# Kernel tuning notes

Hardware: AMD Instinct MI355X
Metric: run time of the kernel (lower is better)

The kernel has to match this reference:

```python
import jax, jax.numpy as jnp
import numpy as np
from jax.scipy.special import logsumexp

T, B, N = 512, 512, 64  # time, batch, labels


def setup_inputs() -> dict:
    key = jax.random.key(0)
    k1, k2, k3, k4, k5, k6 = jax.random.split(key, 6)
    scale = 1.0 / np.sqrt(N).astype(np.float32)  # matches init.normal_(0, 1/sqrt(N))
    emit = jax.random.normal(k1, (T, B, N), jnp.float32)
    transitions = jax.random.normal(k2, (N, N), jnp.float32) * scale
    strans = jax.random.normal(k3, (N,), jnp.float32) * scale
    etrans = jax.random.normal(k4, (N,), jnp.float32) * scale
    target = jax.random.randint(k5, (T, B), 0, N)
    lengths = jax.random.randint(k6, (B,), 1, T + 1)  # at least 1 valid step
    mask = jnp.arange(T)[:, None] < lengths[None, :]  # (T, B) bool, mask[0] all True
    return {"emit": emit, "transitions": transitions, "strans": strans,
            "etrans": etrans, "target": target, "mask": mask}


def reference(emit, transitions, strans, etrans, target, mask):
    # ---- get_logZ: semiring (logsumexp) scan over time ----
    def step(alpha, xs):
        emit_i, mask_i = xs  # (B, N), (B,)
        # scores[b, j] = logsumexp_i alpha[b, i] + trans[i, j] + emit_i[b, j]
        scores = logsumexp(alpha[:, :, None] + transitions[None, :, :]
                           + emit_i[:, None, :], axis=1)
        alpha = jnp.where(mask_i[:, None], scores, alpha)
        return alpha, None

    alpha0 = emit[0] + strans  # (B, N)
    alpha, _ = jax.lax.scan(step, alpha0, (emit[1:], mask[1:]))
    logZ = logsumexp(alpha + etrans, axis=1).sum()

    # ---- score: gold-path score ----
    trans_sc = transitions[target[:-1], target[1:]]                 # (T-1, B)
    emit_sc = jnp.take_along_axis(emit, target[:, :, None], axis=2)[..., 0]  # (T, B)
    step_sc = emit_sc.at[1:].add(trans_sc)
    gold = jnp.where(mask, step_sc, 0.0).sum()
    ends = mask.sum(axis=0) - 1                                     # (B,) last valid step
    gold = gold + strans[target[0]].sum()
    gold = gold + etrans[target[ends, jnp.arange(B)]].sum()

    # negative log-likelihood (standard CRF loss = logZ - gold score)
    return logZ - gold
```

## Files before the change

kernel.cpp:

```cpp
#include <hip/hip_runtime.h>

#define TT 512
#define BB 512
#define NN 64
#define LN2F 0.69314718055994530942f

typedef _Float16 half8_t __attribute__((ext_vector_type(8)));
typedef float    f32x4   __attribute__((ext_vector_type(4)));

union AFrag { int u[4]; half8_t h; };

__device__ __forceinline__ float wave_max(float v) {
    #pragma unroll
    for (int off = 32; off > 0; off >>= 1)
        v = fmaxf(v, __shfl_xor(v, off, 64));
    return v;
}

__device__ __forceinline__ float wave_sum(float v) {
    #pragma unroll
    for (int off = 32; off > 0; off >>= 1)
        v += __shfl_xor(v, off, 64);
    return v;
}

__device__ __forceinline__ int wave_sum_i(int v) {
    #pragma unroll
    for (int off = 32; off > 0; off >>= 1)
        v += __shfl_xor(v, off, 64);
    return v;
}

__device__ __forceinline__ float bcast_lane(float v, int lane) {
    return __uint_as_float(__builtin_amdgcn_readlane(__float_as_uint(v), lane));
}

__device__ __forceinline__ void async4(const float* g, float* l) {
    __builtin_amdgcn_global_load_lds(
        (const __attribute__((address_space(1))) unsigned int*)g,
        (__attribute__((address_space(3))) unsigned int*)l,
        4, 0, 0);
}

__global__ void zero_kernel(float* __restrict__ out) {
    if (threadIdx.x == 0 && blockIdx.x == 0) out[0] = 0.0f;
}

__global__ __launch_bounds__(64) void crf_fwd_kernel(
    const float* __restrict__ emit,
    const float* __restrict__ trans,
    const float* __restrict__ strans,
    const float* __restrict__ etrans,
    const int*   __restrict__ target,
    const void*  __restrict__ maskp,
    float* __restrict__ out)
{
    const int b = blockIdx.x;
    const int k = threadIdx.x;

    __shared__ float sem[2][8][NN];

    const int*           mi32 = (const int*)maskp;
    const unsigned char* mi8  = (const unsigned char*)maskp;
    const bool bytemode = (mi32[0] == 0x01010101);

    int cnt = 0;
    #pragma unroll
    for (int i = 0; i < TT / 64; ++i) {
        const size_t tb = (size_t)(i * 64 + k) * BB + b;
        cnt += bytemode ? (mi8[tb] != 0) : (mi32[tb] != 0);
    }
    const int len = wave_sum_i(cnt);

    const int q   = k >> 4;
    const int nlo = k & 15;
    const bool bit4 = (k & 16) != 0;
    const bool bit5 = (k & 32) != 0;

    const float* ecol = emit + (size_t)b * NN + k;

    #pragma unroll
    for (int s = 0; s < 8; ++s)
        async4(ecol + (size_t)(1 + s) * BB * NN, &sem[0][s][0]);

    half8_t Bf[4][2];
    #pragma unroll
    for (int g = 0; g < 4; ++g) {
        #pragma unroll
        for (int kh = 0; kh < 2; ++kh) {
            AFrag bf;
            #pragma unroll
            for (int jp = 0; jp < 4; ++jp) {
                const int krow = 32 * kh + 8 * q + 2 * jp;
                const float e0 = 0.25f * __expf(trans[(krow + 0) * NN + 16 * g + nlo]);
                const float e1 = 0.25f * __expf(trans[(krow + 1) * NN + 16 * g + nlo]);
                bf.u[jp] = __builtin_bit_cast(int, __builtin_amdgcn_cvt_pkrtz(e0, e1));
            }
            Bf[g][kh] = bf.h;
        }
    }

    int addrs[8];
    #pragma unroll
    for (int kh = 0; kh < 2; ++kh)
        #pragma unroll
        for (int r = 0; r < 4; ++r)
            addrs[4 * kh + r] = 128 * kh + 32 * q + 8 * r;

    const f32x4 zero4 = {0.f, 0.f, 0.f, 0.f};

    const float alpha0 = ecol[0] + strans[k];
    const float m0 = bcast_lane(alpha0, 0);
    float u = __expf(alpha0 - m0);
    int e_sum = 0;

    auto do_step = [&](float wloc) {
        const float uo = __int_as_float(
            __builtin_amdgcn_mov_dpp(__float_as_int(u), 0xB1, 0xF, 0xF, true));
        const int pkv = __builtin_bit_cast(int, __builtin_amdgcn_cvt_pkrtz(u, uo));

        AFrag a0f, a1f;
        #pragma unroll
        for (int r = 0; r < 4; ++r) {
            a0f.u[r] = __builtin_amdgcn_ds_bpermute(addrs[r],     pkv);
            a1f.u[r] = __builtin_amdgcn_ds_bpermute(addrs[4 + r], pkv);
        }

        const f32x4 accA0 = __builtin_amdgcn_mfma_f32_16x16x32_f16(a0f.h, Bf[0][0], zero4, 0, 0, 0);
        const f32x4 accA1 = __builtin_amdgcn_mfma_f32_16x16x32_f16(a0f.h, Bf[1][0], zero4, 0, 0, 0);
        const f32x4 accA2 = __builtin_amdgcn_mfma_f32_16x16x32_f16(a0f.h, Bf[2][0], zero4, 0, 0, 0);
        const f32x4 accA3 = __builtin_amdgcn_mfma_f32_16x16x32_f16(a0f.h, Bf[3][0], zero4, 0, 0, 0);
        const f32x4 acc0 = __builtin_amdgcn_mfma_f32_16x16x32_f16(a1f.h, Bf[0][1], accA0, 0, 0, 0);
        const f32x4 acc1 = __builtin_amdgcn_mfma_f32_16x16x32_f16(a1f.h, Bf[1][1], accA1, 0, 0, 0);
        const f32x4 acc2 = __builtin_amdgcn_mfma_f32_16x16x32_f16(a1f.h, Bf[2][1], accA2, 0, 0, 0);
        const f32x4 acc3 = __builtin_amdgcn_mfma_f32_16x16x32_f16(a1f.h, Bf[3][1], accA3, 0, 0, 0);

        const float sLo  = bit4 ? acc1[0] : acc0[0];
        const float sHi  = bit4 ? acc3[0] : acc2[0];
        const float yown = bit5 ? sHi : sLo;

        const int e = (int)((__builtin_amdgcn_readfirstlane(__float_as_uint(yown)) >> 23) & 0xff) - 127 + 4;
        const float y = yown * wloc;
        u = ldexpf(y, -e);
        e_sum += e + 2;
    };

    int t = 1;
    int half = 0;
    for (; t + 8 <= len; t += 8) {
        float v0 = sem[half][0][k], v1 = sem[half][1][k];
        float v2 = sem[half][2][k], v3 = sem[half][3][k];
        float v4 = sem[half][4][k], v5 = sem[half][5][k];
        float v6 = sem[half][6][k], v7 = sem[half][7][k];

        #pragma unroll
        for (int s = 0; s < 8; ++s) {
            const int tf = (t + 8 + s < TT) ? (t + 8 + s) : (TT - 1);
            async4(ecol + (size_t)tf * BB * NN, &sem[half ^ 1][s][0]);
        }

        const float w0 = __expf(v0), w1 = __expf(v1), w2 = __expf(v2), w3 = __expf(v3);
        const float w4 = __expf(v4), w5 = __expf(v5), w6 = __expf(v6), w7 = __expf(v7);
        do_step(w0); do_step(w1); do_step(w2); do_step(w3);
        do_step(w4); do_step(w5); do_step(w6); do_step(w7);

        half ^= 1;
    }

    for (int s = 0; t < len; ++t, ++s)
        do_step(__expf(sem[half][s][k]));

    const float la = __logf(u) + etrans[k];
    const float m2 = wave_max(la);
    const float sm = wave_sum(__expf(la - m2));
    const float logZ_b = m0 + LN2F * (float)e_sum + m2 + __logf(sm);

    int tvals[TT / 64];
    #pragma unroll
    for (int i = 0; i < TT / 64; ++i)
        tvals[i] = target[(size_t)(64 * i + k) * BB + b];

    float g = 0.f;
    int prev_last = 0;
    #pragma unroll
    for (int i = 0; i < TT / 64; ++i) {
        const int tt = 64 * i + k;
        const int tgt = tvals[i];
        int tprev = __shfl_up(tvals[i], 1, 64);
        if (k == 0) tprev = prev_last;
        prev_last = __builtin_amdgcn_readlane(tvals[i], 63);
        if (tt < len) {
            float v = emit[((size_t)tt * BB + b) * NN + tgt];
            v += (tt == 0) ? strans[tgt] : trans[tprev * NN + tgt];
            if (tt == len - 1) v += etrans[tgt];
            g += v;
        }
    }
    g = wave_sum(g);

    if (k == 0) atomicAdd(out, logZ_b - g);
}

extern "C" void kernel_launch(void* const* d_in, const int* in_sizes, int n_in,
                              void* d_out, int out_size, void* d_ws, size_t ws_size,
                              hipStream_t stream) {
    const float* emit   = (const float*)d_in[0];
    const float* trans  = (const float*)d_in[1];
    const float* strans = (const float*)d_in[2];
    const float* etrans = (const float*)d_in[3];
    const int*   target = (const int*)d_in[4];
    const void*  mask   = d_in[5];
    float* out = (float*)d_out;

    hipLaunchKernelGGL(zero_kernel, dim3(1), dim3(64), 0, stream, out);
    hipLaunchKernelGGL(crf_fwd_kernel, dim3(BB), dim3(64), 0, stream,
                       emit, trans, strans, etrans, target, mask, out);
}
```

Baseline: 184.5 us.

## Split CRF forward scan into parallel time chunks with forward/backward MFMA waves

Replaces the sequential 511-step alpha recurrence with 8 time chunks of 64 steps processed concurrently. Each chunk's transfer is evaluated as a matrix-vector product along the MFMA N dimension. A forward wave propagates a real alpha from chunk 0 and ones-vectors for the other chunks, while a backward wave propagates ones through the transposed transitions. The chunks are stitched via ratio-of-inner-products normalization, with an exact tail recompute for short final chunks. Gold-path scoring moves to a third wave so it overlaps the scan. The sequential dependency chain shrinks to roughly 64 steps plus a stitch, at the cost of more compute and a numerical risk from the rank-one stitching approximation, which relies on mixing of the transition matrix.

Measured after the change: 148.5 us. 19.5% less time.

```diff
diff --git a/kernel.cpp b/kernel.cpp
--- a/kernel.cpp
+++ b/kernel.cpp
@@ -4,6 +4,8 @@
 #define BB 512
 #define NN 64
 #define LN2F 0.69314718055994530942f
+#define SCH 64
+#define EXACT_THRESH 32
 
 typedef _Float16 half8_t __attribute__((ext_vector_type(8)));
 typedef float    f32x4   __attribute__((ext_vector_type(4)));
@@ -31,22 +33,11 @@
     return v;
 }
 
-__device__ __forceinline__ float bcast_lane(float v, int lane) {
-    return __uint_as_float(__builtin_amdgcn_readlane(__float_as_uint(v), lane));
-}
-
-__device__ __forceinline__ void async4(const float* g, float* l) {
-    __builtin_amdgcn_global_load_lds(
-        (const __attribute__((address_space(1))) unsigned int*)g,
-        (__attribute__((address_space(3))) unsigned int*)l,
-        4, 0, 0);
-}
-
 __global__ void zero_kernel(float* __restrict__ out) {
     if (threadIdx.x == 0 && blockIdx.x == 0) out[0] = 0.0f;
 }
 
-__global__ __launch_bounds__(64) void crf_fwd_kernel(
+__global__ __launch_bounds__(192) void crf_fwd_kernel(
     const float* __restrict__ emit,
     const float* __restrict__ trans,
     const float* __restrict__ strans,
@@ -55,10 +46,15 @@
     const void*  __restrict__ maskp,
     float* __restrict__ out)
 {
-    const int b = blockIdx.x;
-    const int k = threadIdx.x;
-
-    __shared__ float sem[2][8][NN];
+    const int b   = blockIdx.x;
+    const int tid = threadIdx.x;
+    const int k   = tid & 63;
+    const int wv  = tid >> 6;
+
+    __shared__ float FL[8][NN];
+    __shared__ float RL[8][NN];
+    __shared__ float xbuf[NN];
+    __shared__ int   esF[8], esB[8];
 
     const int*           mi32 = (const int*)maskp;
     const unsigned char* mi8  = (const unsigned char*)maskp;
@@ -72,133 +68,323 @@
     }
     const int len = wave_sum_i(cnt);
 
-    const int q   = k >> 4;
-    const int nlo = k & 15;
-    const bool bit4 = (k & 16) != 0;
-    const bool bit5 = (k & 32) != 0;
-
-    const float* ecol = emit + (size_t)b * NN + k;
-
-    #pragma unroll
-    for (int s = 0; s < 8; ++s)
-        async4(ecol + (size_t)(1 + s) * BB * NN, &sem[0][s][0]);
-
-    half8_t Bf[4][2];
-    #pragma unroll
-    for (int g = 0; g < 4; ++g) {
-        #pragma unroll
-        for (int kh = 0; kh < 2; ++kh) {
-            AFrag bf;
-            #pragma unroll
-            for (int jp = 0; jp < 4; ++jp) {
-                const int krow = 32 * kh + 8 * q + 2 * jp;
-                const float e0 = 0.25f * __expf(trans[(krow + 0) * NN + 16 * g + nlo]);
-                const float e1 = 0.25f * __expf(trans[(krow + 1) * NN + 16 * g + nlo]);
-                bf.u[jp] = __builtin_bit_cast(int, __builtin_amdgcn_cvt_pkrtz(e0, e1));
-            }
-            Bf[g][kh] = bf.h;
-        }
+    const int q    = k >> 4;
+    const int m15  = k & 15;
+    const int base = 8 * (m15 >> 2) + 2 * (m15 & 3);
+
+    const int  Bc    = (len >= 2) ? ((len - 2) / SCH) : 0;
+    const int  sB    = len - (1 + SCH * Bc);
+    const bool exact = (Bc >= 1) && (sB < EXACT_THRESH);
+
+    const f32x4 zero4 = {0.f, 0.f, 0.f, 0.f};
+    float m0loc = 0.f;
+
+    half8_t Af[4][2];
+    float uLo[8], uHi[8];
+
+    if (wv <= 1) {
+        const bool fwd = (wv == 0);
+        const int cF  = m15 & 7;
+        const int t0  = 1 + SCH * cF;
+        const int nst = min(max(len - t0, 0), SCH);
+        const int tLq = t0 + nst - 1;
+
+        #pragma unroll
+        for (int g = 0; g < 4; ++g) {
+            const int nsg = 32 * (g >> 1) + (g & 1) + base;
+            #pragma unroll
+            for (int kh = 0; kh < 2; ++kh) {
+                AFrag af;
+                #pragma unroll
+                for (int jp = 0; jp < 4; ++jp) {
+                    const int krow = 32 * kh + 8 * q + 2 * jp;
+                    float e0, e1;
+                    if (fwd) {
+                        e0 = 0.25f * __expf(trans[(krow + 0) * NN + nsg]);
+                        e1 = 0.25f * __expf(trans[(krow + 1) * NN + nsg]);
+                    } else {
+                        e0 = 0.25f * __expf(trans[nsg * NN + krow + 0]);
+                        e1 = 0.25f * __expf(trans[nsg * NN + krow + 1]);
+                    }
+                    af.u[jp] = __builtin_bit_cast(int, __builtin_amdgcn_cvt_pkrtz(e0, e1));
+                }
+                Af[g][kh] = af.h;
+            }
+        }
+
+        if (fwd) {
+            const float* p0 = emit + (size_t)b * NN;
+            m0loc = p0[0] + strans[0];
+            const f32x4 e0 = *(const f32x4*)(p0 + 8 * q);
+            const f32x4 e1 = *(const f32x4*)(p0 + 8 * q + 4);
+            const f32x4 e2 = *(const f32x4*)(p0 + 32 + 8 * q);
+            const f32x4 e3 = *(const f32x4*)(p0 + 32 + 8 * q + 4);
+            const f32x4 s0 = *(const f32x4*)(strans + 8 * q);
+            const f32x4 s1 = *(const f32x4*)(strans + 8 * q + 4);
+            const f32x4 s2 = *(const f32x4*)(strans + 32 + 8 * q);
+            const f32x4 s3 = *(const f32x4*)(strans + 32 + 8 * q + 4);
+            #pragma unroll
+            for (int j = 0; j < 4; ++j) {
+                uLo[j]     = (m15 == 0) ? __expf(e0[j] + s0[j] - m0loc) : 1.f;
+                uLo[4 + j] = (m15 == 0) ? __expf(e1[j] + s1[j] - m0loc) : 1.f;
+                uHi[j]     = (m15 == 0) ? __expf(e2[j] + s2[j] - m0loc) : 1.f;
+                uHi[4 + j] = (m15 == 0) ? __expf(e3[j] + s3[j] - m0loc) : 1.f;
+            }
+        } else {
+            #pragma unroll
+            for (int j = 0; j < 8; ++j) { uLo[j] = 1.f; uHi[j] = 1.f; }
+        }
+
+        float mx = uLo[0];
+        #pragma unroll
+        for (int j = 1; j < 8; ++j) mx = fmaxf(mx, uLo[j]);
+        #pragma unroll
+        for (int j = 0; j < 8; ++j) mx = fmaxf(mx, uHi[j]);
+        mx = fmaxf(mx, __shfl_xor(mx, 16, 64));
+        mx = fmaxf(mx, __shfl_xor(mx, 32, 64));
+        int   d  = (int)((__float_as_uint(mx) >> 23) & 0xff) - 127 + 4;
+        float sD = __int_as_float((127 - d) << 23);
+        int   e_acc = 0;
+
+        AFrag BF0, BF1;
+        #pragma unroll
+        for (int r = 0; r < 4; ++r) {
+            BF0.u[r] = __builtin_bit_cast(int, __builtin_amdgcn_cvt_pkrtz(uLo[2 * r], uLo[2 * r + 1]));
+            BF1.u[r] = __builtin_bit_cast(int, __builtin_amdgcn_cvt_pkrtz(uHi[2 * r], uHi[2 * r + 1]));
+        }
+
+        float sLo[8], sHi[8];
+        int   eSnap = 0;
+        #pragma unroll
+        for (int j = 0; j < 8; ++j) { sLo[j] = uLo[j]; sHi[j] = uHi[j]; }
+
+        auto rowOf = [&](int j) -> int {
+            int r = fwd ? (t0 + j) : (tLq - j);
+            r = r < 0 ? 0 : (r > TT - 1 ? TT - 1 : r);
+            return r;
+        };
+        auto LDW = [&](int j, f32x4& r0, f32x4& r1, f32x4& r2, f32x4& r3) {
+            const int rr = rowOf(j);
+            const float* p = emit + ((size_t)rr * BB + b) * NN;
+            r0 = *(const f32x4*)(p + 8 * q);
+            r1 = *(const f32x4*)(p + 8 * q + 4);
+            r2 = *(const f32x4*)(p + 32 + 8 * q);
+            r3 = *(const f32x4*)(p + 32 + 8 * q + 4);
+        };
+        auto SNAP = [&]() {
+            #pragma unroll
+            for (int j = 0; j < 8; ++j) { sLo[j] = uLo[j]; sHi[j] = uHi[j]; }
+            eSnap = e_acc;
+        };
+
+        auto STEP = [&](f32x4& r0, f32x4& r1, f32x4& r2, f32x4& r3, int jn) {
+            float wt0[8], wt1[8];
+            #pragma unroll
+            for (int jj = 0; jj < 4; ++jj) {
+                wt0[jj]     = __expf(r0[jj]) * sD;
+                wt0[4 + jj] = __expf(r1[jj]) * sD;
+                wt1[jj]     = __expf(r2[jj]) * sD;
+                wt1[4 + jj] = __expf(r3[jj]) * sD;
+            }
+            LDW(jn, r0, r1, r2, r3);
+
+            int pf;
+            if (fwd) {
+                const f32x4 aA0 = __builtin_amdgcn_mfma_f32_16x16x32_f16(Af[0][0], BF0.h, zero4, 0, 0, 0);
+                const f32x4 aA1 = __builtin_amdgcn_mfma_f32_16x16x32_f16(Af[1][0], BF0.h, zero4, 0, 0, 0);
+                const f32x4 aA2 = __builtin_amdgcn_mfma_f32_16x16x32_f16(Af[2][0], BF0.h, zero4, 0, 0, 0);
+                const f32x4 aA3 = __builtin_amdgcn_mfma_f32_16x16x32_f16(Af[3][0], BF0.h, zero4, 0, 0, 0);
+                const f32x4 ac0 = __builtin_amdgcn_mfma_f32_16x16x32_f16(Af[0][1], BF1.h, aA0, 0, 0, 0);
+                const f32x4 ac1 = __builtin_amdgcn_mfma_f32_16x16x32_f16(Af[1][1], BF1.h, aA1, 0, 0, 0);
+                const f32x4 ac2 = __builtin_amdgcn_mfma_f32_16x16x32_f16(Af[2][1], BF1.h, aA2, 0, 0, 0);
+                const f32x4 ac3 = __builtin_amdgcn_mfma_f32_16x16x32_f16(Af[3][1], BF1.h, aA3, 0, 0, 0);
+                pf = __builtin_amdgcn_ds_bpermute(m15 << 2, __builtin_bit_cast(int, ac0[0]));
+                #pragma unroll
+                for (int r = 0; r < 4; ++r) {
+                    uLo[2 * r]     = ac0[r] * wt0[2 * r];
+                    uLo[2 * r + 1] = ac1[r] * wt0[2 * r + 1];
+                    uHi[2 * r]     = ac2[r] * wt1[2 * r];
+                    uHi[2 * r + 1] = ac3[r] * wt1[2 * r + 1];
+                }
+                #pragma unroll
+                for (int r = 0; r < 4; ++r) {
+                    BF0.u[r] = __builtin_bit_cast(int, __builtin_amdgcn_cvt_pkrtz(uLo[2 * r], uLo[2 * r + 1]));
+                    BF1.u[r] = __builtin_bit_cast(int, __builtin_amdgcn_cvt_pkrtz(uHi[2 * r], uHi[2 * r + 1]));
+                }
+            } else {
+                float v0[8], v1[8];
+                #pragma unroll
+                for (int j = 0; j < 8; ++j) { v0[j] = uLo[j] * wt0[j]; v1[j] = uHi[j] * wt1[j]; }
+                #pragma unroll
+                for (int r = 0; r < 4; ++r) {
+                    BF0.u[r] = __builtin_bit_cast(int, __builtin_amdgcn_cvt_pkrtz(v0[2 * r], v0[2 * r + 1]));
+                    BF1.u[r] = __builtin_bit_cast(int, __builtin_amdgcn_cvt_pkrtz(v1[2 * r], v1[2 * r + 1]));
+                }
+                const f32x4 aA0 = __builtin_amdgcn_mfma_f32_16x16x32_f16(Af[0][0], BF0.h, zero4, 0, 0, 0);
+                const f32x4 aA1 = __builtin_amdgcn_mfma_f32_16x16x32_f16(Af[1][0], BF0.h, zero4, 0, 0, 0);
+                const f32x4 aA2 = __builtin_amdgcn_mfma_f32_16x16x32_f16(Af[2][0], BF0.h, zero4, 0, 0, 0);
+                const f32x4 aA3 = __builtin_amdgcn_mfma_f32_16x16x32_f16(Af[3][0], BF0.h, zero4, 0, 0, 0);
+                const f32x4 ac0 = __builtin_amdgcn_mfma_f32_16x16x32_f16(Af[0][1], BF1.h, aA0, 0, 0, 0);
+                const f32x4 ac1 = __builtin_amdgcn_mfma_f32_16x16x32_f16(Af[1][1], BF1.h, aA1, 0, 0, 0);
+                const f32x4 ac2 = __builtin_amdgcn_mfma_f32_16x16x32_f16(Af[2][1], BF1.h, aA2, 0, 0, 0);
+                const f32x4 ac3 = __builtin_amdgcn_mfma_f32_16x16x32_f16(Af[3][1], BF1.h, aA3, 0, 0, 0);
+                pf = __builtin_amdgcn_ds_bpermute(m15 << 2, __builtin_bit_cast(int, ac0[0]));
+                #pragma unroll
+                for (int r = 0; r < 4; ++r) {
+                    uLo[2 * r]     = ac0[r];
+                    uLo[2 * r + 1] = ac1[r];
+                    uHi[2 * r]     = ac2[r];
+                    uHi[2 * r + 1] = ac3[r];
+                }
+            }
+            e_acc += d + 2;
+            d  = ((pf >> 23) & 0xff) - 127 + 4;
+            sD = __int_as_float((127 - d) << 23);
+        };
+
+        f32x4 a0, a1, a2, a3, b0, b1, b2, b3;
+        LDW(0, a0, a1, a2, a3);
+        LDW(1, b0, b1, b2, b3);
+        #pragma unroll 1
+        for (int i = 0; i < SCH; i += 2) {
+            if (i == sB) SNAP();
+            STEP(a0, a1, a2, a3, min(i + 2, SCH - 1));
+            if (i + 1 == sB) SNAP();
+            STEP(b0, b1, b2, b3, min(i + 3, SCH - 1));
+        }
+        if (sB == SCH) SNAP();
+
+        if (m15 < 8) {
+            const bool us = (m15 == Bc);
+            float* dst = fwd ? &FL[m15][0] : &RL[m15][0];
+            f32x4 w0, w1, w2, w3;
+            #pragma unroll
+            for (int j = 0; j < 4; ++j) {
+                w0[j] = us ? sLo[j]     : uLo[j];
+                w1[j] = us ? sLo[4 + j] : uLo[4 + j];
+                w2[j] = us ? sHi[j]     : uHi[j];
+                w3[j] = us ? sHi[4 + j] : uHi[4 + j];
+            }
+            *(f32x4*)(dst + 8 * q)          = w0;
+            *(f32x4*)(dst + 8 * q + 4)      = w1;
+            *(f32x4*)(dst + 32 + 8 * q)     = w2;
+            *(f32x4*)(dst + 32 + 8 * q + 4) = w3;
+            if (q == 0) (fwd ? esF : esB)[m15] = us ? eSnap : e_acc;
+        }
+    } else {
+        int tvals[TT / 64];
+        #pragma unroll
+        for (int i = 0; i < TT / 64; ++i)
+            tvals[i] = target[(size_t)(64 * i + k) * BB + b];
+
+        float g = 0.f;
+        int prev_last = 0;
+        #pragma unroll
+        for (int i = 0; i < TT / 64; ++i) {
+            const int tt = 64 * i + k;
+            const int tgt = tvals[i];
+            int tprev = __shfl_up(tvals[i], 1, 64);
+            if (k == 0) tprev = prev_last;
+            prev_last = __builtin_amdgcn_readlane(tvals[i], 63);
+            if (tt < len) {
+                float v = emit[((size_t)tt * BB + b) * NN + tgt];
+                v += (tt == 0) ? strans[tgt] : trans[tprev * NN + tgt];
+                if (tt == len - 1) v += etrans[tgt];
+                g += v;
+            }
+        }
+        g = wave_sum(g);
+        if (k == 0) atomicAdd(out, -g);
     }
 
-    int addrs[8];
-    #pragma unroll
-    for (int kh = 0; kh < 2; ++kh)
-        #pragma unroll
-        for (int r = 0; r < 4; ++r)
-            addrs[4 * kh + r] = 128 * kh + 32 * q + 8 * r;
-
-    const f32x4 zero4 = {0.f, 0.f, 0.f, 0.f};
-
-    const float alpha0 = ecol[0] + strans[k];
-    const float m0 = bcast_lane(alpha0, 0);
-    float u = __expf(alpha0 - m0);
-    int e_sum = 0;
-
-    auto do_step = [&](float wloc) {
-        const float uo = __int_as_float(
-            __builtin_amdgcn_mov_dpp(__float_as_int(u), 0xB1, 0xF, 0xF, true));
-        const int pkv = __builtin_bit_cast(int, __builtin_amdgcn_cvt_pkrtz(u, uo));
-
-        AFrag a0f, a1f;
-        #pragma unroll
-        for (int r = 0; r < 4; ++r) {
-            a0f.u[r] = __builtin_amdgcn_ds_bpermute(addrs[r],     pkv);
-            a1f.u[r] = __builtin_amdgcn_ds_bpermute(addrs[4 + r], pkv);
-        }
-
-        const f32x4 accA0 = __builtin_amdgcn_mfma_f32_16x16x32_f16(a0f.h, Bf[0][0], zero4, 0, 0, 0);
-        const f32x4 accA1 = __builtin_amdgcn_mfma_f32_16x16x32_f16(a0f.h, Bf[1][0], zero4, 0, 0, 0);
-        const f32x4 accA2 = __builtin_amdgcn_mfma_f32_16x16x32_f16(a0f.h, Bf[2][0], zero4, 0, 0, 0);
-        const f32x4 accA3 = __builtin_amdgcn_mfma_f32_16x16x32_f16(a0f.h, Bf[3][0], zero4, 0, 0, 0);
-        const f32x4 acc0 = __builtin_amdgcn_mfma_f32_16x16x32_f16(a1f.h, Bf[0][1], accA0, 0, 0, 0);
-        const f32x4 acc1 = __builtin_amdgcn_mfma_f32_16x16x32_f16(a1f.h, Bf[1][1], accA1, 0, 0, 0);
-        const f32x4 acc2 = __builtin_amdgcn_mfma_f32_16x16x32_f16(a1f.h, Bf[2][1], accA2, 0, 0, 0);
-        const f32x4 acc3 = __builtin_amdgcn_mfma_f32_16x16x32_f16(a1f.h, Bf[3][1], accA3, 0, 0, 0);
-
-        const float sLo  = bit4 ? acc1[0] : acc0[0];
-        const float sHi  = bit4 ? acc3[0] : acc2[0];
-        const float yown = bit5 ? sHi : sLo;
-
-        const int e = (int)((__builtin_amdgcn_readfirstlane(__float_as_uint(yown)) >> 23) & 0xff) - 127 + 4;
-        const float y = yown * wloc;
-        u = ldexpf(y, -e);
-        e_sum += e + 2;
-    };
-
-    int t = 1;
-    int half = 0;
-    for (; t + 8 <= len; t += 8) {
-        float v0 = sem[half][0][k], v1 = sem[half][1][k];
-        float v2 = sem[half][2][k], v3 = sem[half][3][k];
-        float v4 = sem[half][4][k], v5 = sem[half][5][k];
-        float v6 = sem[half][6][k], v7 = sem[half][7][k];
-
-        #pragma unroll
-        for (int s = 0; s < 8; ++s) {
-            const int tf = (t + 8 + s < TT) ? (t + 8 + s) : (TT - 1);
-            async4(ecol + (size_t)tf * BB * NN, &sem[half ^ 1][s][0]);
-        }
-
-        const float w0 = __expf(v0), w1 = __expf(v1), w2 = __expf(v2), w3 = __expf(v3);
-        const float w4 = __expf(v4), w5 = __expf(v5), w6 = __expf(v6), w7 = __expf(v7);
-        do_step(w0); do_step(w1); do_step(w2); do_step(w3);
-        do_step(w4); do_step(w5); do_step(w6); do_step(w7);
-
-        half ^= 1;
+    __syncthreads();
+
+    if (wv == 0) {
+        float x    = FL[0][k];
+        float Ltot = LN2F * (float)esF[0];
+        const int Cend = exact ? (Bc - 1) : Bc;
+
+        for (int c = 1; c <= Cend; ++c) {
+            const float num = wave_sum(RL[c][k] * x);
+            const float den = wave_sum(FL[c][k]);
+            Ltot += __logf(num / den) + LN2F * (float)esB[c];
+            x = FL[c][k];
+        }
+
+        if (exact) {
+            xbuf[k] = x;
+            asm volatile("" ::: "memory");
+            float vLo[8], vHi[8];
+            #pragma unroll
+            for (int j = 0; j < 8; ++j) {
+                vLo[j] = xbuf[8 * q + j];
+                vHi[j] = xbuf[32 + 8 * q + j];
+            }
+            AFrag B0, B1;
+            #pragma unroll
+            for (int r = 0; r < 4; ++r) {
+                B0.u[r] = __builtin_bit_cast(int, __builtin_amdgcn_cvt_pkrtz(vLo[2 * r], vLo[2 * r + 1]));
+                B1.u[r] = __builtin_bit_cast(int, __builtin_amdgcn_cvt_pkrtz(vHi[2 * r], vHi[2 * r + 1]));
+            }
+            int eR = 0;
+            const int t0B = 1 + SCH * Bc;
+            #pragma unroll 1
+            for (int j = 0; j < sB; ++j) {
+                const int rr = t0B + j;
+                const float* p = emit + ((size_t)rr * BB + b) * NN;
+                const f32x4 r0 = *(const f32x4*)(p + 8 * q);
+                const f32x4 r1 = *(const f32x4*)(p + 8 * q + 4);
+                const f32x4 r2 = *(const f32x4*)(p + 32 + 8 * q);
+                const f32x4 r3 = *(const f32x4*)(p + 32 + 8 * q + 4);
+                float wt0[8], wt1[8];
+                #pragma unroll
+                for (int jj = 0; jj < 4; ++jj) {
+                    wt0[jj]     = __expf(r0[jj]);
+                    wt0[4 + jj] = __expf(r1[jj]);
+                    wt1[jj]     = __expf(r2[jj]);
+                    wt1[4 + jj] = __expf(r3[jj]);
+                }
+                const f32x4 aA0 = __builtin_amdgcn_mfma_f32_16x16x32_f16(Af[0][0], B0.h, zero4, 0, 0, 0);
+                const f32x4 aA1 = __builtin_amdgcn_mfma_f32_16x16x32_f16(Af[1][0], B0.h, zero4, 0, 0, 0);
+                const f32x4 aA2 = __builtin_amdgcn_mfma_f32_16x16x32_f16(Af[2][0], B0.h, zero4, 0, 0, 0);
+                const f32x4 aA3 = __builtin_amdgcn_mfma_f32_16x16x32_f16(Af[3][0], B0.h, zero4, 0, 0, 0);
+                const f32x4 ac0 = __builtin_amdgcn_mfma_f32_16x16x32_f16(Af[0][1], B1.h, aA0, 0, 0, 0);
+                const f32x4 ac1 = __builtin_amdgcn_mfma_f32_16x16x32_f16(Af[1][1], B1.h, aA1, 0, 0, 0);
+                const f32x4 ac2 = __builtin_amdgcn_mfma_f32_16x16x32_f16(Af[2][1], B1.h, aA2, 0, 0, 0);
+                const f32x4 ac3 = __builtin_amdgcn_mfma_f32_16x16x32_f16(Af[3][1], B1.h, aA3, 0, 0, 0);
+                const int e = (int)((__builtin_amdgcn_readfirstlane(__float_as_uint(ac0[0])) >> 23) & 0xff) - 127 + 4;
+                const float sE = __int_as_float((127 - e) << 23);
+                #pragma unroll
+                for (int r = 0; r < 4; ++r) {
+                    vLo[2 * r]     = ac0[r] * wt0[2 * r]     * sE;
+                    vLo[2 * r + 1] = ac1[r] * wt0[2 * r + 1] * sE;
+                    vHi[2 * r]     = ac2[r] * wt1[2 * r]     * sE;
+                    vHi[2 * r + 1] = ac3[r] * wt1[2 * r + 1] * sE;
+                }
+                #pragma unroll
+                for (int r = 0; r < 4; ++r) {
+                    B0.u[r] = __builtin_bit_cast(int, __builtin_amdgcn_cvt_pkrtz(vLo[2 * r], vLo[2 * r + 1]));
+                    B1.u[r] = __builtin_bit_cast(int, __builtin_amdgcn_cvt_pkrtz(vHi[2 * r], vHi[2 * r + 1]));
+                }
+                eR += e + 2;
+            }
+            asm volatile("" ::: "memory");
+            *(f32x4*)&xbuf[8 * q]          = *(f32x4*)&vLo[0];
+            *(f32x4*)&xbuf[8 * q + 4]      = *(f32x4*)&vLo[4];
+            *(f32x4*)&xbuf[32 + 8 * q]     = *(f32x4*)&vHi[0];
+            *(f32x4*)&xbuf[32 + 8 * q + 4] = *(f32x4*)&vHi[4];
+            asm volatile("" ::: "memory");
+            x = xbuf[k];
+            Ltot += LN2F * (float)eR;
+        }
+
+        const float la = __logf(x) + etrans[k];
+        const float m2 = wave_max(la);
+        const float sm = wave_sum(__expf(la - m2));
+        const float logZ_b = m0loc + Ltot + m2 + __logf(sm);
+
+        if (k == 0) atomicAdd(out, logZ_b);
     }
-
-    for (int s = 0; t < len; ++t, ++s)
-        do_step(__expf(sem[half][s][k]));
-
-    const float la = __logf(u) + etrans[k];
-    const float m2 = wave_max(la);
-    const float sm = wave_sum(__expf(la - m2));
-    const float logZ_b = m0 + LN2F * (float)e_sum + m2 + __logf(sm);
-
-    int tvals[TT / 64];
-    #pragma unroll
-    for (int i = 0; i < TT / 64; ++i)
-        tvals[i] = target[(size_t)(64 * i + k) * BB + b];
-
-    float g = 0.f;
-    int prev_last = 0;
-    #pragma unroll
-    for (int i = 0; i < TT / 64; ++i) {
-        const int tt = 64 * i + k;
-        const int tgt = tvals[i];
-        int tprev = __shfl_up(tvals[i], 1, 64);
-        if (k == 0) tprev = prev_last;
-        prev_last = __builtin_amdgcn_readlane(tvals[i], 63);
-        if (tt < len) {
-            float v = emit[((size_t)tt * BB + b) * NN + tgt];
-            v += (tt == 0) ? strans[tgt] : trans[tprev * NN + tgt];
-            if (tt == len - 1) v += etrans[tgt];
-            g += v;
-        }
-    }
-    g = wave_sum(g);
-
-    if (k == 0) atomicAdd(out, logZ_b - g);
 }
 
 extern "C" void kernel_launch(void* const* d_in, const int* in_sizes, int n_in,
@@ -213,6 +399,6 @@
     float* out = (float*)d_out;
 
     hipLaunchKernelGGL(zero_kernel, dim3(1), dim3(64), 0, stream, out);
-    hipLaunchKernelGGL(crf_fwd_kernel, dim3(BB), dim3(64), 0, stream,
+    hipLaunchKernelGGL(crf_fwd_kernel, dim3(BB), dim3(192), 0, stream,
                        emit, trans, strans, etrans, target, mask, out);
 }
```
